# Optimization experiments

Measured on AMD Instinct MI355X. Metric: run time of the kernel, lower is better.

## Reference

```python
import jax, jax.numpy as jnp
import numpy as np

N_HEADS, D_MODEL, D_HEAD = 16, 1024, 64
INIT_STD = 0.02
IGNORE = -100000.0


def setup_inputs() -> dict:
    key = jax.random.key(0)
    ks = jax.random.split(key, 5)
    x = jax.random.normal(ks[0], (2, 2048, D_MODEL), dtype=jnp.float32)
    W_Q = INIT_STD * jax.random.normal(ks[1], (N_HEADS, D_MODEL, D_HEAD), dtype=jnp.float32)
    W_K = INIT_STD * jax.random.normal(ks[2], (N_HEADS, D_MODEL, D_HEAD), dtype=jnp.float32)
    W_V = INIT_STD * jax.random.normal(ks[3], (N_HEADS, D_MODEL, D_HEAD), dtype=jnp.float32)
    W_O = INIT_STD * jax.random.normal(ks[4], (N_HEADS, D_HEAD, D_MODEL), dtype=jnp.float32)
    b_Q = jnp.zeros((N_HEADS, D_HEAD), dtype=jnp.float32)
    b_K = jnp.zeros((N_HEADS, D_HEAD), dtype=jnp.float32)
    b_V = jnp.zeros((N_HEADS, D_HEAD), dtype=jnp.float32)
    b_O = jnp.zeros((D_MODEL,), dtype=jnp.float32)
    return {"normalized_resid_pre": x, "W_Q": W_Q, "W_K": W_K, "W_V": W_V,
            "W_O": W_O, "b_Q": b_Q, "b_K": b_K, "b_V": b_V, "b_O": b_O}


def reference(normalized_resid_pre, W_Q, W_K, W_V, W_O, b_Q, b_K, b_V, b_O):
    x = normalized_resid_pre  # [b, s, d_model]
    q = jnp.einsum('bsm,hmd->bshd', x, W_Q) + b_Q  # [b, s, h, d_head]
    k = jnp.einsum('bsm,hmd->bshd', x, W_K) + b_K
    v = jnp.einsum('bsm,hmd->bshd', x, W_V) + b_V
    scores = jnp.einsum('bqhd,bkhd->bhqk', q, k) / jnp.sqrt(jnp.float32(D_HEAD))
    s = x.shape[1]
    causal = jnp.triu(jnp.ones((s, s), dtype=bool), k=1)  # True above diagonal
    scores = jnp.where(causal, jnp.float32(IGNORE), scores)
    pattern = jax.nn.softmax(scores, axis=-1)  # [b, h, q, k]
    z = jnp.einsum('bkhd,bhqk->bqhd', v, pattern)
    attn_out = jnp.einsum('bqhd,hdm->bqm', z, W_O) + b_O
    return attn_out
```

## Files before the change

### kernel.cpp

```cpp
#include <hip/hip_runtime.h>
#include <hip/hip_bf16.h>

#define BB   2
#define SS   2048
#define HH   16
#define DM_  1024
#define DH_  64
#define NROW 4096
#define NQKV 3072

typedef unsigned short u16;
typedef unsigned int u32;
using short4v = __attribute__((ext_vector_type(4))) short;
using short8 = __attribute__((ext_vector_type(8))) short;
using bf16x8 = __attribute__((ext_vector_type(8))) __bf16;
using f32x4  = __attribute__((ext_vector_type(4))) float;
using f32x16 = __attribute__((ext_vector_type(16))) float;

#define QSCALE 0.180336880f

__device__ __forceinline__ u16 f2bf(float f) {
    union { float f; unsigned u; } v; v.f = f;
    unsigned r = v.u + 0x7fffu + ((v.u >> 16) & 1u);
    return (u16)(r >> 16);
}

__device__ __forceinline__ f32x4 mfma16(bf16x8 a, bf16x8 b, f32x4 c) {
    return __builtin_amdgcn_mfma_f32_16x16x32_bf16(a, b, c, 0, 0, 0);
}
__device__ __forceinline__ f32x16 mfma32(bf16x8 a, bf16x8 b, f32x16 c) {
    return __builtin_amdgcn_mfma_f32_32x32x16_bf16(a, b, c, 0, 0, 0);
}

__device__ __forceinline__ u32 cvtpk(float lo, float hi) {
    u32 r;
    asm("v_cvt_pk_bf16_f32 %0, %1, %2" : "=v"(r) : "v"(lo), "v"(hi));
    return r;
}
#define PLSWAP(a, b) asm("v_permlane32_swap_b32 %0, %1" : "+v"(a), "+v"(b))

__device__ __forceinline__ float fexp2(float x) {
#if __has_builtin(__builtin_amdgcn_exp2f)
    return __builtin_amdgcn_exp2f(x);
#else
    float r; asm("v_exp_f32 %0, %1" : "=v"(r) : "v"(x)); return r;
#endif
}

__device__ __forceinline__ void gload16(const void* g, void* l) {
    __builtin_amdgcn_global_load_lds(
        (const __attribute__((address_space(1))) void*)g,
        (__attribute__((address_space(3))) void*)l, 16, 0, 0);
}

__global__ __launch_bounds__(256)
void prep(const float* __restrict__ x,  const float* __restrict__ wq,
          const float* __restrict__ wk, const float* __restrict__ wv,
          const float* __restrict__ wo, const float* __restrict__ bq,
          const float* __restrict__ bk, const float* __restrict__ bv,
          u16* __restrict__ Xb, u16* __restrict__ Wt,
          u16* __restrict__ WoT, float* __restrict__ biasQKV) {
    __shared__ float tile[64][65];
    const int bx = blockIdx.x, t = threadIdx.x;
    if (bx < 512) {
        const int tid = bx * 256 + t;
        #pragma unroll
        for (int it = 0; it < 8; ++it) {
            int i = tid + it * 131072;
            float4 v = ((const float4*)x)[i];
            u16 b4[4] = {f2bf(v.x), f2bf(v.y), f2bf(v.z), f2bf(v.w)};
            ((short4v*)Xb)[i] = *(short4v*)b4;
        }
        if (tid < NQKV) {
            int mat = tid >> 10, h = (tid >> 6) & 15, d = tid & 63;
            const float* bb = (mat == 0) ? bq : ((mat == 1) ? bk : bv);
            biasQKV[tid] = bb[h * DH_ + d];
        }
    } else if (bx < 1280) {
        const int idx = bx - 512;
        const int m0 = (idx & 15) * 64, hm = idx >> 4;
        const int mat = hm >> 4, h = hm & 15;
        const float* w = (mat == 0) ? wq : ((mat == 1) ? wk : wv);
        #pragma unroll
        for (int it = 0; it < 4; ++it) {
            int row = it * 16 + (t >> 4), c4 = (t & 15) * 4;
            float4 v = *(const float4*)&w[((size_t)h * 1024 + m0 + row) * 64 + c4];
            tile[row][c4] = v.x; tile[row][c4 + 1] = v.y;
            tile[row][c4 + 2] = v.z; tile[row][c4 + 3] = v.w;
        }
        __syncthreads();
        #pragma unroll
        for (int it = 0; it < 2; ++it) {
            int c = it * 256 + t, d = c >> 3, mc = (c & 7) * 8;
            u16 buf[8];
            #pragma unroll
            for (int j = 0; j < 8; ++j) buf[j] = f2bf(tile[mc + j][d]);
            *(short8*)&Wt[((size_t)(mat * 1024 + h * 64 + d)) * 1024 + m0 + mc] = *(short8*)buf;
        }
    } else {
        const int idx = bx - 1280;
        const int n0 = (idx & 15) * 64, k0 = (idx >> 4) * 64;
        #pragma unroll
        for (int it = 0; it < 4; ++it) {
            int row = it * 16 + (t >> 4), c4 = (t & 15) * 4;
            float4 v = *(const float4*)&wo[(size_t)(k0 + row) * DM_ + n0 + c4];
            tile[row][c4] = v.x; tile[row][c4 + 1] = v.y;
            tile[row][c4 + 2] = v.z; tile[row][c4 + 3] = v.w;
        }
        __syncthreads();
        #pragma unroll
        for (int it = 0; it < 2; ++it) {
            int c = it * 256 + t, n = c >> 3, kc = (c & 7) * 8;
            u16 buf[8];
            #pragma unroll
            for (int j = 0; j < 8; ++j) buf[j] = f2bf(tile[kc + j][n]);
            *(short8*)&WoT[(size_t)(n0 + n) * DM_ + k0 + kc] = *(short8*)buf;
        }
    }
}

__device__ __forceinline__ void gemm_core_128(
    const u16* __restrict__ Ap, const u16* __restrict__ Bp,
    int brow, int bcol, u16* lds, f32x4 acc[4][2]) {
    const int t = threadIdx.x, l = t & 63;
    const int wid = t >> 6, wm = wid >> 2, wn = wid & 3;
    const int c0 = t, c1 = t + 512;
    const int r0 = c0 >> 3, sb0 = ((c0 & 7) ^ (r0 & 7)) << 3;
    const int r1 = c1 >> 3, sb1 = ((c1 & 7) ^ (r1 & 7)) << 3;
    u16* A0 = lds;
    u16* B0 = lds + 16384;
    const int rA0 = wm * 64 + (l & 15);
    const int rB0 = wn * 32 + (l & 15);
    const int sw  = (l & 7) << 3;
    const int colA = ((l >> 4) << 3);

    {
        gload16(Ap + (size_t)(brow + r0) * DM_ + sb0, A0 + c0 * 8);
        gload16(Ap + (size_t)(brow + r1) * DM_ + sb1, A0 + c1 * 8);
        gload16(Bp + (size_t)(bcol + r0) * DM_ + sb0, B0 + c0 * 8);
        gload16(Bp + (size_t)(bcol + r1) * DM_ + sb1, B0 + c1 * 8);
    }
    __syncthreads();
    for (int kt = 0; kt < 16; ++kt) {
        const int p = kt & 1;
        if (kt < 15) {
            const int ko = (kt + 1) * 64;
            gload16(Ap + (size_t)(brow + r0) * DM_ + ko + sb0, A0 + (p ^ 1) * 8192 + c0 * 8);
            gload16(Ap + (size_t)(brow + r1) * DM_ + ko + sb1, A0 + (p ^ 1) * 8192 + c1 * 8);
            gload16(Bp + (size_t)(bcol + r0) * DM_ + ko + sb0, B0 + (p ^ 1) * 8192 + c0 * 8);
            gload16(Bp + (size_t)(bcol + r1) * DM_ + ko + sb1, B0 + (p ^ 1) * 8192 + c1 * 8);
        }
        const u16* Ab = A0 + p * 8192;
        const u16* Bb = B0 + p * 8192;
        #pragma unroll
        for (int kc = 0; kc < 64; kc += 32) {
            const int cx = (kc + colA) ^ sw;
            bf16x8 af[4], bfr[2];
            #pragma unroll
            for (int m = 0; m < 4; ++m)
                af[m] = *(const bf16x8*)(Ab + (rA0 + m * 16) * 64 + cx);
            #pragma unroll
            for (int n = 0; n < 2; ++n)
                bfr[n] = *(const bf16x8*)(Bb + (rB0 + n * 16) * 64 + cx);
            __builtin_amdgcn_s_setprio(1);
            #pragma unroll
            for (int m = 0; m < 4; ++m)
                #pragma unroll
                for (int n = 0; n < 2; ++n)
                    acc[m][n] = mfma16(af[m], bfr[n], acc[m][n]);
            __builtin_amdgcn_s_setprio(0);
        }
        __syncthreads();
    }
}

__global__ __launch_bounds__(512)
void gemm_qkv3(const u16* __restrict__ Xb, const u16* __restrict__ Wt,
               const float* __restrict__ bias, u16* __restrict__ Qs,
               u16* __restrict__ Ks, u16* __restrict__ Vt) {
    __shared__ __align__(16) u16 lds[32768];
    const int bx = blockIdx.x, t = threadIdx.x, l = t & 63;
    const int wid = t >> 6, wm = wid >> 2, wn = wid & 3;
    f32x4 acc[4][2] = {};
    const bool isV = (bx >= 512);
    int brow, bcol; const u16 *Ap, *Bp;
    if (!isV) { brow = (bx & 31) * 128; bcol = (bx >> 5) * 128; Ap = Xb; Bp = Wt; }
    else { int i2 = bx - 512; brow = (i2 & 7) * 128; bcol = (i2 >> 3) * 128;
           Ap = Wt + (size_t)2048 * DM_; Bp = Xb; }
    gemm_core_128(Ap, Bp, brow, bcol, lds, acc);

    u16* wr_ = lds + wid * 2048;
    const int colbase = bcol + wn * 32;
    const int rowbase = brow + wm * 64;
    const int rsub = ((l >> 4) << 2);
    if (!isV) {
        const float b0 = bias[colbase + (l & 15)];
        const float b1 = bias[colbase + 16 + (l & 15)];
        const float scl = (colbase < 1024) ? QSCALE : 1.0f;
        #pragma unroll
        for (int m = 0; m < 4; ++m)
            #pragma unroll
            for (int n = 0; n < 2; ++n) {
                const float bb = n ? b1 : b0;
                #pragma unroll
                for (int r = 0; r < 4; ++r)
                    wr_[(m * 16 + rsub + r) * 32 + n * 16 + (l & 15)] =
                        f2bf((acc[m][n][r] + bb) * scl);
            }
    } else {
        #pragma unroll
        for (int m = 0; m < 4; ++m) {
            float4 bv = *(const float4*)&bias[2048 + rowbase + m * 16 + rsub];
            const float bbr[4] = {bv.x, bv.y, bv.z, bv.w};
            #pragma unroll
            for (int n = 0; n < 2; ++n)
                #pragma unroll
                for (int r = 0; r < 4; ++r)
                    wr_[(m * 16 + rsub + r) * 32 + n * 16 + (l & 15)] =
                        f2bf(acc[m][n][r] + bbr[r]);
        }
    }
    __syncthreads();
    if (!isV) {
        const int hsel = (colbase >> 6) & 15, d0 = colbase & 63;
        const int bsel = rowbase >> 11, s0 = rowbase & 2047;
        u16* outp = (colbase < 1024) ? Qs : Ks;
        #pragma unroll
        for (int p = 0; p < 4; ++p) {
            const int rr = p * 16 + (l >> 2);
            short8 v = *(const short8*)(wr_ + rr * 32 + (l & 3) * 8);
            *(short8*)&outp[(((size_t)bsel * HH + hsel) * SS + s0 + rr) * DH_ + d0 + (l & 3) * 8] = v;
        }
    } else {
        const int bsel = colbase >> 11, s0 = colbase & 2047;
        #pragma unroll
        for (int p = 0; p < 4; ++p) {
            const int rr = p * 16 + (l >> 2);
            short8 v = *(const short8*)(wr_ + rr * 32 + (l & 3) * 8);
            *(short8*)&Vt[((size_t)bsel * 1024 + rowbase + rr) * SS + s0 + (l & 3) * 8] = v;
        }
    }
}

__global__ __launch_bounds__(512)
void gemm_out3(const u16* __restrict__ Zb, const u16* __restrict__ WoT,
               const float* __restrict__ bO, float* __restrict__ out) {
    __shared__ __align__(16) u16 lds[32768];
    const int bx = blockIdx.x, t = threadIdx.x, l = t & 63;
    const int wid = t >> 6, wm = wid >> 2, wn = wid & 3;
    const int brow = (bx & 31) * 128, bcol = (bx >> 5) * 128;
    f32x4 acc[4][2] = {};
    gemm_core_128(Zb, WoT, brow, bcol, lds, acc);
    const int colbase = bcol + wn * 32;
    const int rowbase = brow + wm * 64;
    const int rsub = ((l >> 4) << 2);
    const float b0 = bO[colbase + (l & 15)];
    const float b1 = bO[colbase + 16 + (l & 15)];
    #pragma unroll
    for (int m = 0; m < 4; ++m)
        #pragma unroll
        for (int n = 0; n < 2; ++n) {
            const float bb = n ? b1 : b0;
            #pragma unroll
            for (int r = 0; r < 4; ++r)
                out[(size_t)(rowbase + m * 16 + rsub + r) * DM_ + colbase + n * 16 + (l & 15)] =
                    acc[m][n][r] + bb;
        }
}

__global__ __launch_bounds__(512, 4)
void attn_fwd(const u16* __restrict__ Qs, const u16* __restrict__ Ks,
              const u16* __restrict__ Vt, u16* __restrict__ Zb) {
    __shared__ __align__(16) u16 fK[2][8192];
    __shared__ __align__(16) u16 fV[2][8192];
    __shared__ float lrP[128];
    __shared__ float lrX[128];
    const int bidx = blockIdx.x;
    const int j  = (bidx < 256) ? (15 - (bidx >> 5)) : ((bidx - 256) >> 5);
    const int bh = bidx & 31, b = bh >> 4, h = bh & 15;
    const int t = threadIdx.x, wid = t >> 6, l = t & 63;
    const int hi = l >> 5, c32 = l & 31;
    const int qh = wid >> 1, par = wid & 1;
    const u16* Qp = Qs + (size_t)bh * SS * DH_;
    const u16* Kp = Ks + (size_t)bh * SS * DH_;
    const u16* Vp = Vt + (size_t)bh * DH_ * SS;
    const int qw = j * 128 + qh * 32;
    const int nr = j + 1;

    bf16x8 aq[4];
    #pragma unroll
    for (int dk = 0; dk < 4; ++dk)
        aq[dk] = *(const bf16x8*)&Qp[(size_t)(qw + c32) * DH_ + dk * 16 + hi * 8];

    int kOff[2]; size_t vOff[2]; int dstc[2];
    #pragma unroll
    for (int i = 0; i < 2; ++i) {
        const int c = t + 512 * i, sec = c >> 6, ln = c & 63;
        const int kh = sec >> 3, s7 = sec & 7;
        kOff[i] = (kh * 64 + (s7 >> 2) * 32 + (ln & 31)) * DH_ + (s7 & 3) * 16 + (ln >> 5) * 8;
        vOff[i] = (size_t)((s7 >> 2) * 32 + (ln & 31)) * SS + kh * 64 + (s7 & 3) * 16 + (ln >> 5) * 8;
        dstc[i] = c * 8;
    }

    #define ISSUE(rr, pb)                                                     \
    {   const int ka = (rr) * 128;                                            \
        gload16(Kp + (size_t)ka * DH_ + kOff[0], &fK[pb][dstc[0]]);           \
        gload16(Kp + (size_t)ka * DH_ + kOff[1], &fK[pb][dstc[1]]);           \
        gload16(Vp + ka + vOff[0], &fV[pb][dstc[0]]);                         \
        gload16(Vp + ka + vOff[1], &fV[pb][dstc[1]]);                         \
    }

    ISSUE(0, 0)
    __syncthreads();

    f32x16 o0 = {}, o1 = {};
    float lrp[4] = {0.f, 0.f, 0.f, 0.f};

    for (int r = 0; r < nr; ++r) {
        const int p = r & 1;
        if (r + 1 < nr) ISSUE(r + 1, p ^ 1)
        const int kv0 = r * 128 + par * 64;
        if (kv0 <= qw + 31) {
            const u16* fKb = &fK[p][par * 4096];
            const u16* fVb = &fV[p][par * 4096];
            const bool have1 = (kv0 + 32 <= qw + 31);
            f32x16 s0 = {}, s1 = {};
            #pragma unroll
            for (int dk = 0; dk < 4; ++dk)
                s0 = mfma32(*(const bf16x8*)(fKb + dk * 512 + l * 8), aq[dk], s0);
            if (have1) {
                #pragma unroll
                for (int dk = 0; dk < 4; ++dk)
                    s1 = mfma32(*(const bf16x8*)(fKb + (4 + dk) * 512 + l * 8), aq[dk], s1);
            }
            if (kv0 + 63 > qw) {
                const int q = qw + c32;
                #pragma unroll
                for (int r16 = 0; r16 < 16; ++r16) {
                    const int crow = (r16 & 3) + 8 * (r16 >> 2) + 4 * hi;
                    if (kv0 + crow > q) s0[r16] = -1e30f;
                }
                if (have1) {
                    #pragma unroll
                    for (int r16 = 0; r16 < 16; ++r16) {
                        const int crow = (r16 & 3) + 8 * (r16 >> 2) + 4 * hi;
                        if (kv0 + 32 + crow > q) s1[r16] = -1e30f;
                    }
                }
            }
            #pragma unroll
            for (int r16 = 0; r16 < 16; ++r16) {
                s0[r16] = fexp2(s0[r16]);
                lrp[r16 & 3] += s0[r16];
            }
            if (have1) {
                #pragma unroll
                for (int r16 = 0; r16 < 16; ++r16) {
                    s1[r16] = fexp2(s1[r16]);
                    lrp[r16 & 3] += s1[r16];
                }
            }
            #define PV_STEP(PS, B8, KS)                                          \
            {                                                                    \
                u32 cA  = cvtpk(PS[B8 + 0], PS[B8 + 1]);                         \
                u32 cA2 = cvtpk(PS[B8 + 2], PS[B8 + 3]);                         \
                u32 cB  = cvtpk(PS[B8 + 4], PS[B8 + 5]);                         \
                u32 cB2 = cvtpk(PS[B8 + 6], PS[B8 + 7]);                         \
                PLSWAP(cA, cB); PLSWAP(cA2, cB2);                                \
                u32 w[4] = {cA, cA2, cB, cB2};                                   \
                bf16x8 pa = *(bf16x8*)w;                                         \
                o0 = mfma32(pa, *(const bf16x8*)(fVb + (0 * 4 + (KS)) * 512 + l * 8), o0); \
                o1 = mfma32(pa, *(const bf16x8*)(fVb + (1 * 4 + (KS)) * 512 + l * 8), o1); \
            }
            PV_STEP(s0, 0, 0)
            PV_STEP(s0, 8, 1)
            if (have1) {
                PV_STEP(s1, 0, 2)
                PV_STEP(s1, 8, 3)
            }
            #undef PV_STEP
        }
        __syncthreads();
    }
    #undef ISSUE

    float lrow = (lrp[0] + lrp[1]) + (lrp[2] + lrp[3]);
    lrow += __shfl_xor(lrow, 32);

    float* mrg = (float*)fK;
    __syncthreads();
    if (par) {
        #pragma unroll
        for (int e = 0; e < 16; ++e) mrg[qh * 2048 + e * 64 + l] = o0[e];
        #pragma unroll
        for (int e = 0; e < 16; ++e) mrg[qh * 2048 + (16 + e) * 64 + l] = o1[e];
        if (hi == 0) lrP[qh * 32 + c32] = lrow;
    }
    __syncthreads();
    if (!par) {
        #pragma unroll
        for (int e = 0; e < 16; ++e) o0[e] += mrg[qh * 2048 + e * 64 + l];
        #pragma unroll
        for (int e = 0; e < 16; ++e) o1[e] += mrg[qh * 2048 + (16 + e) * 64 + l];
        lrow += lrP[qh * 32 + c32];
        lrX[qh * 32 + c32] = lrow;
        float invv[16];
        #pragma unroll
        for (int g = 0; g < 4; ++g) {
            float4 lv = *(const float4*)&lrX[qh * 32 + 8 * g + 4 * hi];
            invv[g * 4 + 0] = 1.0f / lv.x;
            invv[g * 4 + 1] = 1.0f / lv.y;
            invv[g * 4 + 2] = 1.0f / lv.z;
            invv[g * 4 + 3] = 1.0f / lv.w;
        }
        #pragma unroll
        for (int r16 = 0; r16 < 16; ++r16) {
            const int q = qw + (r16 & 3) + 8 * (r16 >> 2) + 4 * hi;
            u16* zp = &Zb[(((size_t)b * SS + q) * HH + h) * DH_];
            zp[c32]      = f2bf(o0[r16] * invv[r16]);
            zp[32 + c32] = f2bf(o1[r16] * invv[r16]);
        }
    }
}

extern "C" void kernel_launch(void* const* d_in, const int* in_sizes, int n_in,
                              void* d_out, int out_size, void* d_ws, size_t ws_size,
                              hipStream_t stream) {
    const float* x  = (const float*)d_in[0];
    const float* wq = (const float*)d_in[1];
    const float* wk = (const float*)d_in[2];
    const float* wv = (const float*)d_in[3];
    const float* wo = (const float*)d_in[4];
    const float* bq = (const float*)d_in[5];
    const float* bk = (const float*)d_in[6];
    const float* bv = (const float*)d_in[7];
    const float* bO = (const float*)d_in[8];
    float* out = (float*)d_out;

    char* w = (char*)d_ws;
    u16* Xb  = (u16*)w;  w += (size_t)NROW * DM_ * 2;
    u16* Wt  = (u16*)w;  w += (size_t)NQKV * DM_ * 2;
    u16* WoT = (u16*)w;  w += (size_t)DM_ * DM_ * 2;
    float* biasQKV = (float*)w; w += (size_t)NQKV * 4;
    u16* Qs  = (u16*)w;  w += (size_t)BB * HH * SS * DH_ * 2;
    u16* Ks  = (u16*)w;  w += (size_t)BB * HH * SS * DH_ * 2;
    u16* Vt  = (u16*)w;  w += (size_t)BB * HH * SS * DH_ * 2;
    u16* Zb  = (u16*)w;  w += (size_t)BB * HH * SS * DH_ * 2;

    prep<<<1536, 256, 0, stream>>>(x, wq, wk, wv, wo, bq, bk, bv,
                                   Xb, Wt, WoT, biasQKV);
    gemm_qkv3<<<768, 512, 0, stream>>>(Xb, Wt, biasQKV, Qs, Ks, Vt);
    attn_fwd<<<512, 512, 0, stream>>>(Qs, Ks, Vt, Zb);
    gemm_out3<<<256, 512, 0, stream>>>(Zb, WoT, bO, out);
}
```

Before: 94.81 us.

## Process 64 query rows per wave in attention to reuse K/V fragments

Halves the attention block to 4 waves, and each wave now computes two 32-row query tiles. Each K and V fragment read from shared memory is applied to both tiles, which cuts LDS traffic per MFMA. Each thread also issues twice as many global-to-LDS loads. The cost is more accumulator registers per wave and fewer waves per block, which lowers the parallelism available for latency hiding.

```diff
diff --git a/kernel.cpp b/kernel.cpp
--- a/kernel.cpp
+++ b/kernel.cpp
@@ -268,7 +268,7 @@
         }
 }
 
-__global__ __launch_bounds__(512, 4)
+__global__ __launch_bounds__(256, 2)
 void attn_fwd(const u16* __restrict__ Qs, const u16* __restrict__ Ks,
               const u16* __restrict__ Vt, u16* __restrict__ Zb) {
     __shared__ __align__(16) u16 fK[2][8192];
@@ -284,18 +284,20 @@
     const u16* Qp = Qs + (size_t)bh * SS * DH_;
     const u16* Kp = Ks + (size_t)bh * SS * DH_;
     const u16* Vp = Vt + (size_t)bh * DH_ * SS;
-    const int qw = j * 128 + qh * 32;
+    const int qw = j * 128 + qh * 64;
     const int nr = j + 1;
 
-    bf16x8 aq[4];
+    bf16x8 aq0[4], aq1[4];
     #pragma unroll
-    for (int dk = 0; dk < 4; ++dk)
-        aq[dk] = *(const bf16x8*)&Qp[(size_t)(qw + c32) * DH_ + dk * 16 + hi * 8];
-
-    int kOff[2]; size_t vOff[2]; int dstc[2];
+    for (int dk = 0; dk < 4; ++dk) {
+        aq0[dk] = *(const bf16x8*)&Qp[(size_t)(qw + c32) * DH_ + dk * 16 + hi * 8];
+        aq1[dk] = *(const bf16x8*)&Qp[(size_t)(qw + 32 + c32) * DH_ + dk * 16 + hi * 8];
+    }
+
+    int kOff[4]; size_t vOff[4]; int dstc[4];
     #pragma unroll
-    for (int i = 0; i < 2; ++i) {
-        const int c = t + 512 * i, sec = c >> 6, ln = c & 63;
+    for (int i = 0; i < 4; ++i) {
+        const int c = t + 256 * i, sec = c >> 6, ln = c & 63;
         const int kh = sec >> 3, s7 = sec & 7;
         kOff[i] = (kh * 64 + (s7 >> 2) * 32 + (ln & 31)) * DH_ + (s7 & 3) * 16 + (ln >> 5) * 8;
         vOff[i] = (size_t)((s7 >> 2) * 32 + (ln & 31)) * SS + kh * 64 + (s7 & 3) * 16 + (ln >> 5) * 8;
@@ -306,119 +308,158 @@
     {   const int ka = (rr) * 128;                                            \
         gload16(Kp + (size_t)ka * DH_ + kOff[0], &fK[pb][dstc[0]]);           \
         gload16(Kp + (size_t)ka * DH_ + kOff[1], &fK[pb][dstc[1]]);           \
+        gload16(Kp + (size_t)ka * DH_ + kOff[2], &fK[pb][dstc[2]]);           \
+        gload16(Kp + (size_t)ka * DH_ + kOff[3], &fK[pb][dstc[3]]);           \
         gload16(Vp + ka + vOff[0], &fV[pb][dstc[0]]);                         \
         gload16(Vp + ka + vOff[1], &fV[pb][dstc[1]]);                         \
+        gload16(Vp + ka + vOff[2], &fV[pb][dstc[2]]);                         \
+        gload16(Vp + ka + vOff[3], &fV[pb][dstc[3]]);                         \
     }
 
     ISSUE(0, 0)
     __syncthreads();
 
-    f32x16 o0 = {}, o1 = {};
-    float lrp[4] = {0.f, 0.f, 0.f, 0.f};
+    f32x16 o00 = {}, o01 = {}, o10 = {}, o11 = {};
+    float lrp0[4] = {0.f, 0.f, 0.f, 0.f};
+    float lrp1[4] = {0.f, 0.f, 0.f, 0.f};
 
     for (int r = 0; r < nr; ++r) {
         const int p = r & 1;
         if (r + 1 < nr) ISSUE(r + 1, p ^ 1)
         const int kv0 = r * 128 + par * 64;
-        if (kv0 <= qw + 31) {
+        if (kv0 <= qw + 63) {
             const u16* fKb = &fK[p][par * 4096];
             const u16* fVb = &fV[p][par * 4096];
-            const bool have1 = (kv0 + 32 <= qw + 31);
-            f32x16 s0 = {}, s1 = {};
-            #pragma unroll
-            for (int dk = 0; dk < 4; ++dk)
-                s0 = mfma32(*(const bf16x8*)(fKb + dk * 512 + l * 8), aq[dk], s0);
-            if (have1) {
-                #pragma unroll
-                for (int dk = 0; dk < 4; ++dk)
-                    s1 = mfma32(*(const bf16x8*)(fKb + (4 + dk) * 512 + l * 8), aq[dk], s1);
-            }
-            if (kv0 + 63 > qw) {
-                const int q = qw + c32;
-                #pragma unroll
-                for (int r16 = 0; r16 < 16; ++r16) {
-                    const int crow = (r16 & 3) + 8 * (r16 >> 2) + 4 * hi;
-                    if (kv0 + crow > q) s0[r16] = -1e30f;
-                }
-                if (have1) {
+            #pragma unroll
+            for (int kg = 0; kg < 2; ++kg) {
+                const int kb = kv0 + kg * 32;
+                if (kb > qw + 63) continue;
+                const bool nd0 = (kb <= qw + 31);
+                f32x16 sA = {}, sB = {};
+                #pragma unroll
+                for (int dk = 0; dk < 4; ++dk) {
+                    bf16x8 kf = *(const bf16x8*)(fKb + (kg * 4 + dk) * 512 + l * 8);
+                    if (nd0) sA = mfma32(kf, aq0[dk], sA);
+                    sB = mfma32(kf, aq1[dk], sB);
+                }
+                if (nd0 && kb + 31 > qw) {
+                    const int q = qw + c32;
                     #pragma unroll
                     for (int r16 = 0; r16 < 16; ++r16) {
                         const int crow = (r16 & 3) + 8 * (r16 >> 2) + 4 * hi;
-                        if (kv0 + 32 + crow > q) s1[r16] = -1e30f;
+                        if (kb + crow > q) sA[r16] = -1e30f;
                     }
                 }
+                if (kb + 31 > qw + 32) {
+                    const int q = qw + 32 + c32;
+                    #pragma unroll
+                    for (int r16 = 0; r16 < 16; ++r16) {
+                        const int crow = (r16 & 3) + 8 * (r16 >> 2) + 4 * hi;
+                        if (kb + crow > q) sB[r16] = -1e30f;
+                    }
+                }
+                if (nd0) {
+                    #pragma unroll
+                    for (int r16 = 0; r16 < 16; ++r16) {
+                        sA[r16] = fexp2(sA[r16]);
+                        lrp0[r16 & 3] += sA[r16];
+                    }
+                }
+                #pragma unroll
+                for (int r16 = 0; r16 < 16; ++r16) {
+                    sB[r16] = fexp2(sB[r16]);
+                    lrp1[r16 & 3] += sB[r16];
+                }
+                #pragma unroll
+                for (int h8 = 0; h8 < 2; ++h8) {
+                    const int KS = kg * 2 + h8;
+                    const int B8 = h8 * 8;
+                    bf16x8 v0 = *(const bf16x8*)(fVb + (0 * 4 + KS) * 512 + l * 8);
+                    bf16x8 v1 = *(const bf16x8*)(fVb + (1 * 4 + KS) * 512 + l * 8);
+                    if (nd0) {
+                        u32 cA  = cvtpk(sA[B8 + 0], sA[B8 + 1]);
+                        u32 cA2 = cvtpk(sA[B8 + 2], sA[B8 + 3]);
+                        u32 cB  = cvtpk(sA[B8 + 4], sA[B8 + 5]);
+                        u32 cB2 = cvtpk(sA[B8 + 6], sA[B8 + 7]);
+                        PLSWAP(cA, cB); PLSWAP(cA2, cB2);
+                        u32 w0[4] = {cA, cA2, cB, cB2};
+                        bf16x8 pa = *(bf16x8*)w0;
+                        o00 = mfma32(pa, v0, o00);
+                        o01 = mfma32(pa, v1, o01);
+                    }
+                    {
+                        u32 cA  = cvtpk(sB[B8 + 0], sB[B8 + 1]);
+                        u32 cA2 = cvtpk(sB[B8 + 2], sB[B8 + 3]);
+                        u32 cB  = cvtpk(sB[B8 + 4], sB[B8 + 5]);
+                        u32 cB2 = cvtpk(sB[B8 + 6], sB[B8 + 7]);
+                        PLSWAP(cA, cB); PLSWAP(cA2, cB2);
+                        u32 w1[4] = {cA, cA2, cB, cB2};
+                        bf16x8 pa = *(bf16x8*)w1;
+                        o10 = mfma32(pa, v0, o10);
+                        o11 = mfma32(pa, v1, o11);
+                    }
+                }
             }
-            #pragma unroll
-            for (int r16 = 0; r16 < 16; ++r16) {
-                s0[r16] = fexp2(s0[r16]);
-                lrp[r16 & 3] += s0[r16];
-            }
-            if (have1) {
-                #pragma unroll
-                for (int r16 = 0; r16 < 16; ++r16) {
-                    s1[r16] = fexp2(s1[r16]);
-                    lrp[r16 & 3] += s1[r16];
-                }
-            }
-            #define PV_STEP(PS, B8, KS)                                          \
-            {                                                                    \
-                u32 cA  = cvtpk(PS[B8 + 0], PS[B8 + 1]);                         \
-                u32 cA2 = cvtpk(PS[B8 + 2], PS[B8 + 3]);                         \
-                u32 cB  = cvtpk(PS[B8 + 4], PS[B8 + 5]);                         \
-                u32 cB2 = cvtpk(PS[B8 + 6], PS[B8 + 7]);                         \
-                PLSWAP(cA, cB); PLSWAP(cA2, cB2);                                \
-                u32 w[4] = {cA, cA2, cB, cB2};                                   \
-                bf16x8 pa = *(bf16x8*)w;                                         \
-                o0 = mfma32(pa, *(const bf16x8*)(fVb + (0 * 4 + (KS)) * 512 + l * 8), o0); \
-                o1 = mfma32(pa, *(const bf16x8*)(fVb + (1 * 4 + (KS)) * 512 + l * 8), o1); \
-            }
-            PV_STEP(s0, 0, 0)
-            PV_STEP(s0, 8, 1)
-            if (have1) {
-                PV_STEP(s1, 0, 2)
-                PV_STEP(s1, 8, 3)
-            }
-            #undef PV_STEP
         }
         __syncthreads();
     }
     #undef ISSUE
 
-    float lrow = (lrp[0] + lrp[1]) + (lrp[2] + lrp[3]);
-    lrow += __shfl_xor(lrow, 32);
+    float lrow0 = (lrp0[0] + lrp0[1]) + (lrp0[2] + lrp0[3]);
+    float lrow1 = (lrp1[0] + lrp1[1]) + (lrp1[2] + lrp1[3]);
+    lrow0 += __shfl_xor(lrow0, 32);
+    lrow1 += __shfl_xor(lrow1, 32);
 
     float* mrg = (float*)fK;
     __syncthreads();
+    const int rg0 = (qh * 2 + 0) * 2048, rg1 = (qh * 2 + 1) * 2048;
     if (par) {
         #pragma unroll
-        for (int e = 0; e < 16; ++e) mrg[qh * 2048 + e * 64 + l] = o0[e];
-        #pragma unroll
-        for (int e = 0; e < 16; ++e) mrg[qh * 2048 + (16 + e) * 64 + l] = o1[e];
-        if (hi == 0) lrP[qh * 32 + c32] = lrow;
+        for (int e = 0; e < 16; ++e) mrg[rg0 + e * 64 + l] = o00[e];
+        #pragma unroll
+        for (int e = 0; e < 16; ++e) mrg[rg0 + (16 + e) * 64 + l] = o01[e];
+        #pragma unroll
+        for (int e = 0; e < 16; ++e) mrg[rg1 + e * 64 + l] = o10[e];
+        #pragma unroll
+        for (int e = 0; e < 16; ++e) mrg[rg1 + (16 + e) * 64 + l] = o11[e];
+        if (hi == 0) {
+            lrP[(qh * 2 + 0) * 32 + c32] = lrow0;
+            lrP[(qh * 2 + 1) * 32 + c32] = lrow1;
+        }
     }
     __syncthreads();
     if (!par) {
         #pragma unroll
-        for (int e = 0; e < 16; ++e) o0[e] += mrg[qh * 2048 + e * 64 + l];
-        #pragma unroll
-        for (int e = 0; e < 16; ++e) o1[e] += mrg[qh * 2048 + (16 + e) * 64 + l];
-        lrow += lrP[qh * 32 + c32];
-        lrX[qh * 32 + c32] = lrow;
-        float invv[16];
+        for (int e = 0; e < 16; ++e) o00[e] += mrg[rg0 + e * 64 + l];
+        #pragma unroll
+        for (int e = 0; e < 16; ++e) o01[e] += mrg[rg0 + (16 + e) * 64 + l];
+        #pragma unroll
+        for (int e = 0; e < 16; ++e) o10[e] += mrg[rg1 + e * 64 + l];
+        #pragma unroll
+        for (int e = 0; e < 16; ++e) o11[e] += mrg[rg1 + (16 + e) * 64 + l];
+        lrow0 += lrP[(qh * 2 + 0) * 32 + c32];
+        lrow1 += lrP[(qh * 2 + 1) * 32 + c32];
+        lrX[(qh * 2 + 0) * 32 + c32] = lrow0;
+        lrX[(qh * 2 + 1) * 32 + c32] = lrow1;
+        float inv0[16], inv1[16];
         #pragma unroll
         for (int g = 0; g < 4; ++g) {
-            float4 lv = *(const float4*)&lrX[qh * 32 + 8 * g + 4 * hi];
-            invv[g * 4 + 0] = 1.0f / lv.x;
-            invv[g * 4 + 1] = 1.0f / lv.y;
-            invv[g * 4 + 2] = 1.0f / lv.z;
-            invv[g * 4 + 3] = 1.0f / lv.w;
+            float4 lv0 = *(const float4*)&lrX[(qh * 2 + 0) * 32 + 8 * g + 4 * hi];
+            float4 lv1 = *(const float4*)&lrX[(qh * 2 + 1) * 32 + 8 * g + 4 * hi];
+            inv0[g * 4 + 0] = 1.0f / lv0.x; inv0[g * 4 + 1] = 1.0f / lv0.y;
+            inv0[g * 4 + 2] = 1.0f / lv0.z; inv0[g * 4 + 3] = 1.0f / lv0.w;
+            inv1[g * 4 + 0] = 1.0f / lv1.x; inv1[g * 4 + 1] = 1.0f / lv1.y;
+            inv1[g * 4 + 2] = 1.0f / lv1.z; inv1[g * 4 + 3] = 1.0f / lv1.w;
         }
         #pragma unroll
         for (int r16 = 0; r16 < 16; ++r16) {
-            const int q = qw + (r16 & 3) + 8 * (r16 >> 2) + 4 * hi;
-            u16* zp = &Zb[(((size_t)b * SS + q) * HH + h) * DH_];
-            zp[c32]      = f2bf(o0[r16] * invv[r16]);
-            zp[32 + c32] = f2bf(o1[r16] * invv[r16]);
+            const int crow = (r16 & 3) + 8 * (r16 >> 2) + 4 * hi;
+            u16* zp0 = &Zb[(((size_t)b * SS + (qw + crow)) * HH + h) * DH_];
+            u16* zp1 = &Zb[(((size_t)b * SS + (qw + 32 + crow)) * HH + h) * DH_];
+            zp0[c32]      = f2bf(o00[r16] * inv0[r16]);
+            zp0[32 + c32] = f2bf(o01[r16] * inv0[r16]);
+            zp1[c32]      = f2bf(o10[r16] * inv1[r16]);
+            zp1[32 + c32] = f2bf(o11[r16] * inv1[r16]);
         }
     }
 }
@@ -450,6 +491,6 @@
     prep<<<1536, 256, 0, stream>>>(x, wq, wk, wv, wo, bq, bk, bv,
                                    Xb, Wt, WoT, biasQKV);
     gemm_qkv3<<<768, 512, 0, stream>>>(Xb, Wt, biasQKV, Qs, Ks, Vt);
-    attn_fwd<<<512, 512, 0, stream>>>(Qs, Ks, Vt, Zb);
+    attn_fwd<<<512, 256, 0, stream>>>(Qs, Ks, Vt, Zb);
     gemm_out3<<<256, 512, 0, stream>>>(Zb, WoT, bO, out);
 }
```

New measurement: 101.4 us. 7.0% more time.
